# Optimization experiments

Measured on AMD Instinct MI355X. Metric: run time of the kernel, lower is better.

Reference implementation:

```python
import jax, jax.numpy as jnp
import numpy as np

N, E, G = 200000, 800000, 8192
IN, H, D, EXTRA = 128, 4, 64, 16


def setup_inputs() -> dict:
    key = jax.random.key(0)
    ks = jax.random.split(key, 24)
    inp = {
        'feats_node': jax.random.normal(ks[0], (N, IN), jnp.float32),
        'feats_graph': jax.random.normal(ks[1], (G, EXTRA), jnp.float32),
        'src': jax.random.randint(ks[2], (E,), 0, N, jnp.int32),
        'dst': jax.random.randint(ks[3], (E,), 0, N, jnp.int32),
        'graph_ids': jnp.sort(jax.random.randint(ks[4], (N,), 0, G, jnp.int32)),
        # GAT layer 1: fc [H*D, IN], attn [H, D], bias zeros (DGL default)
        'fc1_w': 0.5 * jax.random.normal(ks[5], (H * D, IN), jnp.float32),
        'attn_l1': 0.5 * jax.random.normal(ks[6], (H, D), jnp.float32),
        'attn_r1': 0.5 * jax.random.normal(ks[7], (H, D), jnp.float32),
        'bias1': jnp.zeros((H * D,), jnp.float32),
        # GAT layer 2
        'fc2_w': 0.5 * jax.random.normal(ks[8], (H * D, H * D), jnp.float32),
        'attn_l2': 0.5 * jax.random.normal(ks[9], (H, D), jnp.float32),
        'attn_r2': 0.5 * jax.random.normal(ks[10], (H, D), jnp.float32),
        'bias2': jnp.zeros((H * D,), jnp.float32),
        # GAT layer 3: 1 head
        'fc3_w': 0.5 * jax.random.normal(ks[11], (D, H * D), jnp.float32),
        'attn_l3': 0.5 * jax.random.normal(ks[12], (1, D), jnp.float32),
        'attn_r3': 0.5 * jax.random.normal(ks[13], (1, D), jnp.float32),
        'bias3': jnp.zeros((D,), jnp.float32),
        # readout score
        'score_w': 0.5 * jax.random.normal(ks[14], (1, D), jnp.float32),
        'score_b': jnp.zeros((1,), jnp.float32),
        # MLP: [D+EXTRA -> 2D -> D -> 1]
        'mlp_w1': 0.5 * jax.random.normal(ks[15], (2 * D, D + EXTRA), jnp.float32),
        'mlp_b1': jnp.zeros((2 * D,), jnp.float32),
        'mlp_w2': 0.5 * jax.random.normal(ks[16], (D, 2 * D), jnp.float32),
        'mlp_b2': jnp.zeros((D,), jnp.float32),
        'mlp_w3': 0.5 * jax.random.normal(ks[17], (1, D), jnp.float32),
        'mlp_b3': jnp.zeros((1,), jnp.float32),
    }
    return inp


def gat_conv(x, src, dst, fc_w, attn_l, attn_r, bias, n_heads, out_dim):
    # DGL GATConv: proj -> edge leaky_relu attention -> per-dst softmax -> aggregate
    n = x.shape[0]
    feat = (x @ fc_w.T).reshape(n, n_heads, out_dim)          # [N,H,D]
    el = jnp.einsum('nhd,hd->nh', feat, attn_l)               # [N,H]
    er = jnp.einsum('nhd,hd->nh', feat, attn_r)
    e = jax.nn.leaky_relu(el[src] + er[dst], 0.2)             # [E,H]
    m = jax.ops.segment_max(e, dst, num_segments=n)           # per-dst max
    m = jax.lax.stop_gradient(jnp.where(jnp.isfinite(m), m, 0.0))
    a = jnp.exp(e - m[dst])                                   # [E,H]
    denom = jax.ops.segment_sum(a, dst, num_segments=n)       # [N,H]
    alpha = a / jnp.where(denom[dst] == 0, 1.0, denom[dst])
    out = jax.ops.segment_sum(alpha[:, :, None] * feat[src], dst, num_segments=n)
    return out + bias.reshape(1, n_heads, out_dim)            # [N,H,D]


def reference(feats_node, feats_graph, src, dst, graph_ids,
              fc1_w, attn_l1, attn_r1, bias1,
              fc2_w, attn_l2, attn_r2, bias2,
              fc3_w, attn_l3, attn_r3, bias3,
              score_w, score_b,
              mlp_w1, mlp_b1, mlp_w2, mlp_b2, mlp_w3, mlp_b3):
    n = feats_node.shape[0]
    g = feats_graph.shape[0]
    x = jax.nn.selu(gat_conv(feats_node, src, dst, fc1_w, attn_l1, attn_r1, bias1, H, D)).reshape(n, H * D)
    x = jax.nn.selu(gat_conv(x, src, dst, fc2_w, attn_l2, attn_r2, bias2, H, D)).reshape(n, H * D)
    x = jax.nn.selu(gat_conv(x, src, dst, fc3_w, attn_l3, attn_r3, bias3, 1, D)).reshape(n, D)
    # weighted-average readout: sum(w*x)/sum(w) per graph
    w = jax.nn.sigmoid(x @ score_w.T + score_b)               # [N,1]
    num = jax.ops.segment_sum(w * x, graph_ids, num_segments=g)
    den = jax.ops.segment_sum(w, graph_ids, num_segments=g)
    emb = num / jnp.where(den == 0, 1.0, den)                 # [G,D]
    z = jnp.concatenate([emb, feats_graph], axis=1)           # [G,D+EXTRA]
    h = jax.nn.selu(z @ mlp_w1.T + mlp_b1)
    h = jax.nn.selu(h @ mlp_w2.T + mlp_b2)
    return h @ mlp_w3.T + mlp_b3                              # [G,1]
```

## Files before the change

### kernel.cpp

```cpp
#include <hip/hip_runtime.h>
#include <math.h>

#define N_NODES 200000
#define N_EDGES 800000
#define N_GRAPHS 8192
#define B1 16
#define B2G 16
#define EC2 128

typedef unsigned short ushort_t;

__device__ __forceinline__ float selu_f(float x){
  const float alpha = 1.6732632423543772f;
  const float lam   = 1.0507009873554805f;
  return x > 0.f ? lam * x : lam * alpha * (expf(x) - 1.f);
}
__device__ __forceinline__ float dot4(float4 a, float4 b){
  return a.x * b.x + a.y * b.y + a.z * b.z + a.w * b.w;
}

__global__ void zero_i32(int* p, int n){
  int i = blockIdx.x * 256 + threadIdx.x;
  if (i < n) p[i] = 0;
}

__global__ void deg_kernel(const int* __restrict__ dst, int* __restrict__ deg, int E){
  int e = blockIdx.x * 256 + threadIdx.x;
  if (e < E) atomicAdd(&deg[dst[e]], 1);
}

__global__ void scan1(const int* __restrict__ deg, int* __restrict__ rp, int* __restrict__ bs, int n){
  __shared__ int sh[256];
  int t = threadIdx.x;
  int base = blockIdx.x * 1024;
  int v[4]; int s = 0;
  #pragma unroll
  for (int i = 0; i < 4; i++){
    int idx = base + t * 4 + i;
    v[i] = (idx < n) ? deg[idx] : 0;
    s += v[i];
  }
  sh[t] = s; __syncthreads();
  for (int off = 1; off < 256; off <<= 1){
    int x = (t >= off) ? sh[t - off] : 0;
    __syncthreads();
    sh[t] += x;
    __syncthreads();
  }
  int run = (t == 0) ? 0 : sh[t - 1];
  #pragma unroll
  for (int i = 0; i < 4; i++){
    int idx = base + t * 4 + i;
    if (idx < n) rp[idx] = run;
    run += v[i];
  }
  if (t == 255) bs[blockIdx.x] = sh[255];
}

__global__ void scan2(int* bs, int nb){
  __shared__ int sh[256];
  int t = threadIdx.x;
  sh[t] = (t < nb) ? bs[t] : 0; __syncthreads();
  for (int off = 1; off < 256; off <<= 1){
    int x = (t >= off) ? sh[t - off] : 0;
    __syncthreads();
    sh[t] += x;
    __syncthreads();
  }
  int excl = (t == 0) ? 0 : sh[t - 1];
  if (t < nb) bs[t] = excl;
}

__global__ void scan3(int* rp, const int* __restrict__ bs, int n, int total){
  int i = blockIdx.x * 256 + threadIdx.x;
  if (i < n) rp[i] += bs[i >> 10];
  if (i == 0) rp[n] = total;
}

__global__ void fill_csr(const int* __restrict__ src, const int* __restrict__ dst,
                         const int* __restrict__ rp, int* __restrict__ fil,
                         int* __restrict__ csr, int E){
  int e = blockIdx.x * 256 + threadIdx.x;
  if (e < E){
    int d = dst[e];
    int p = atomicAdd(&fil[d], 1);
    csr[rp[d] + p] = src[e];
  }
}

__global__ void compute_v(const float* __restrict__ W1, const float* __restrict__ al1, const float* __restrict__ ar1,
                          const float* __restrict__ W2, const float* __restrict__ al2, const float* __restrict__ ar2,
                          const float* __restrict__ W3, const float* __restrict__ al3, const float* __restrict__ ar3,
                          float* __restrict__ V1L, float* __restrict__ V1R,
                          float* __restrict__ V2L, float* __restrict__ V2R,
                          float* __restrict__ V3L, float* __restrict__ V3R){
  int i = blockIdx.x * 256 + threadIdx.x;
  if (i < 512){
    int h = i >> 7, k = i & 127;
    float sl = 0.f, sr = 0.f;
    for (int dd = 0; dd < 64; dd++){
      float w = W1[(size_t)(h * 64 + dd) * 128 + k];
      sl += al1[h * 64 + dd] * w;
      sr += ar1[h * 64 + dd] * w;
    }
    V1L[i] = sl; V1R[i] = sr;
  } else if (i < 1536){
    int j = i - 512;
    int h = j >> 8, k = j & 255;
    float sl = 0.f, sr = 0.f;
    for (int dd = 0; dd < 64; dd++){
      float w = W2[(size_t)(h * 64 + dd) * 256 + k];
      sl += al2[h * 64 + dd] * w;
      sr += ar2[h * 64 + dd] * w;
    }
    V2L[j] = sl; V2R[j] = sr;
  } else if (i < 1792){
    int k = i - 1536;
    float sl = 0.f, sr = 0.f;
    for (int dd = 0; dd < 64; dd++){
      float w = W3[(size_t)dd * 256 + k];
      sl += al3[dd] * w;
      sr += ar3[dd] * w;
    }
    V3L[k] = sl; V3R[k] = sr;
  }
}

__global__ __launch_bounds__(256) void el_er1(const float* __restrict__ x0,
                                              const float* __restrict__ V1L, const float* __restrict__ V1R,
                                              float* __restrict__ el1, float* __restrict__ er1, int n){
  __shared__ float vl[512], vr[512];
  int t = threadIdx.x;
  for (int i = t; i < 512; i += 256){ vl[i] = V1L[i]; vr[i] = V1R[i]; }
  __syncthreads();
  int node = blockIdx.x * 4 + (t >> 6);
  int l = t & 63;
  if (node >= n) return;
  float xa = x0[(size_t)node * 128 + l];
  float xb = x0[(size_t)node * 128 + 64 + l];
  #pragma unroll
  for (int h = 0; h < 4; h++){
    float pl = xa * vl[h * 128 + l] + xb * vl[h * 128 + 64 + l];
    float pr = xa * vr[h * 128 + l] + xb * vr[h * 128 + 64 + l];
    #pragma unroll
    for (int off = 32; off; off >>= 1){ pl += __shfl_xor(pl, off); pr += __shfl_xor(pr, off); }
    if (l == 0){ el1[(size_t)node * 4 + h] = pl; er1[(size_t)node * 4 + h] = pr; }
  }
}

__global__ __launch_bounds__(256) void alpha_h4(const float* __restrict__ el, const float* __restrict__ er,
                                                const int* __restrict__ rp, const int* __restrict__ csr,
                                                float* __restrict__ a, int n){
  int node = blockIdx.x * 256 + threadIdx.x;
  if (node >= n) return;
  int s0 = rp[node], s1 = rp[node + 1];
  if (s0 >= s1) return;
  float4 erv = *reinterpret_cast<const float4*>(er + (size_t)node * 4);
  float m0 = -1e30f, m1 = -1e30f, m2 = -1e30f, m3 = -1e30f;
  for (int i = s0; i < s1; i++){
    float4 e = *reinterpret_cast<const float4*>(el + (size_t)csr[i] * 4);
    float e0 = e.x + erv.x; e0 = e0 > 0.f ? e0 : 0.2f * e0; m0 = fmaxf(m0, e0);
    float e1 = e.y + erv.y; e1 = e1 > 0.f ? e1 : 0.2f * e1; m1 = fmaxf(m1, e1);
    float e2 = e.z + erv.z; e2 = e2 > 0.f ? e2 : 0.2f * e2; m2 = fmaxf(m2, e2);
    float e3 = e.w + erv.w; e3 = e3 > 0.f ? e3 : 0.2f * e3; m3 = fmaxf(m3, e3);
  }
  float d0 = 0.f, d1 = 0.f, d2 = 0.f, d3 = 0.f;
  for (int i = s0; i < s1; i++){
    float4 e = *reinterpret_cast<const float4*>(el + (size_t)csr[i] * 4);
    float e0 = e.x + erv.x; e0 = e0 > 0.f ? e0 : 0.2f * e0; d0 += expf(e0 - m0);
    float e1 = e.y + erv.y; e1 = e1 > 0.f ? e1 : 0.2f * e1; d1 += expf(e1 - m1);
    float e2 = e.z + erv.z; e2 = e2 > 0.f ? e2 : 0.2f * e2; d2 += expf(e2 - m2);
    float e3 = e.w + erv.w; e3 = e3 > 0.f ? e3 : 0.2f * e3; d3 += expf(e3 - m3);
  }
  d0 = 1.f / d0; d1 = 1.f / d1; d2 = 1.f / d2; d3 = 1.f / d3;
  for (int i = s0; i < s1; i++){
    float4 e = *reinterpret_cast<const float4*>(el + (size_t)csr[i] * 4);
    float4 o;
    float e0 = e.x + erv.x; e0 = e0 > 0.f ? e0 : 0.2f * e0; o.x = expf(e0 - m0) * d0;
    float e1 = e.y + erv.y; e1 = e1 > 0.f ? e1 : 0.2f * e1; o.y = expf(e1 - m1) * d1;
    float e2 = e.z + erv.z; e2 = e2 > 0.f ? e2 : 0.2f * e2; o.z = expf(e2 - m2) * d2;
    float e3 = e.w + erv.w; e3 = e3 > 0.f ? e3 : 0.2f * e3; o.w = expf(e3 - m3) * d3;
    *reinterpret_cast<float4*>(a + (size_t)i * 4) = o;
  }
}

__global__ __launch_bounds__(256) void alpha_h1(const float* __restrict__ el, const float* __restrict__ er,
                                                const int* __restrict__ rp, const int* __restrict__ csr,
                                                float* __restrict__ a, int n){
  int node = blockIdx.x * 256 + threadIdx.x;
  if (node >= n) return;
  int s0 = rp[node], s1 = rp[node + 1];
  if (s0 >= s1) return;
  float erv = er[node];
  float m = -1e30f;
  for (int i = s0; i < s1; i++){
    float e = el[csr[i]] + erv; e = e > 0.f ? e : 0.2f * e; m = fmaxf(m, e);
  }
  float den = 0.f;
  for (int i = s0; i < s1; i++){
    float e = el[csr[i]] + erv; e = e > 0.f ? e : 0.2f * e; den += expf(e - m);
  }
  float inv = 1.f / den;
  for (int i = s0; i < s1; i++){
    float e = el[csr[i]] + erv; e = e > 0.f ? e : 0.2f * e; a[i] = expf(e - m) * inv;
  }
}

__global__ __launch_bounds__(512, 4) void l1_fused(
    const float* __restrict__ x0, const float* __restrict__ W1, const float* __restrict__ bias1,
    const float* __restrict__ a1, const float* __restrict__ W2,
    const float* __restrict__ V2L, const float* __restrict__ V2R,
    const int* __restrict__ rp, const int* __restrict__ csr,
    ushort_t* __restrict__ y1hi, unsigned char* __restrict__ y1lo,
    float* __restrict__ el2, float* __restrict__ er2){
  __shared__ float aggT[4][B1][132];
  __shared__ int rpc[B1 + 1];
  float* x1s = &aggT[0][0][0];
  int t = threadIdx.x;
  int nb0 = blockIdx.x * B1;
  if (t <= B1) rpc[t] = rp[nb0 + t];
  __syncthreads();

  {
    int g = t >> 5, c4 = t & 31;
    int i0 = rpc[g], i1 = rpc[g + 1];
    float acc[4][4] = {{0.f}};
    int s = (i0 < i1) ? csr[i0] : 0;
    for (int i = i0; i < i1; i++){
      int sn = (i + 1 < i1) ? csr[i + 1] : 0;
      float4 av = *reinterpret_cast<const float4*>(a1 + (size_t)i * 4);
      float4 xv = *reinterpret_cast<const float4*>(x0 + (size_t)s * 128 + c4 * 4);
      acc[0][0] += av.x * xv.x; acc[0][1] += av.x * xv.y; acc[0][2] += av.x * xv.z; acc[0][3] += av.x * xv.w;
      acc[1][0] += av.y * xv.x; acc[1][1] += av.y * xv.y; acc[1][2] += av.y * xv.z; acc[1][3] += av.y * xv.w;
      acc[2][0] += av.z * xv.x; acc[2][1] += av.z * xv.y; acc[2][2] += av.z * xv.z; acc[2][3] += av.z * xv.w;
      acc[3][0] += av.w * xv.x; acc[3][1] += av.w * xv.y; acc[3][2] += av.w * xv.z; acc[3][3] += av.w * xv.w;
      s = sn;
    }
    #pragma unroll
    for (int h = 0; h < 4; h++){
      float4 v = make_float4(acc[h][0], acc[h][1], acc[h][2], acc[h][3]);
      *reinterpret_cast<float4*>(&aggT[h][g][c4 * 4]) = v;
    }
  }
  __syncthreads();

  int mq = t >> 3, dg = t & 7;
  int m0 = mq * 4;
  int hh = mq >> 4;

  float acc1[4][2];
  {
    #pragma unroll
    for (int j = 0; j < 4; j++){ acc1[j][0] = 0.f; acc1[j][1] = 0.f; }
    const float* wp = W1 + (size_t)m0 * 128;
    #pragma unroll 2
    for (int kq = 0; kq < 32; kq++){
      int k = kq * 4;
      float4 w0 = *reinterpret_cast<const float4*>(wp + k);
      float4 w1 = *reinterpret_cast<const float4*>(wp + 128 + k);
      float4 w2 = *reinterpret_cast<const float4*>(wp + 256 + k);
      float4 w3 = *reinterpret_cast<const float4*>(wp + 384 + k);
      float4 a0 = *reinterpret_cast<const float4*>(&aggT[hh][dg][k]);
      float4 a1v = *reinterpret_cast<const float4*>(&aggT[hh][dg + 8][k]);
      acc1[0][0] += dot4(w0, a0); acc1[0][1] += dot4(w0, a1v);
      acc1[1][0] += dot4(w1, a0); acc1[1][1] += dot4(w1, a1v);
      acc1[2][0] += dot4(w2, a0); acc1[2][1] += dot4(w2, a1v);
      acc1[3][0] += dot4(w3, a0); acc1[3][1] += dot4(w3, a1v);
    }
  }
  __syncthreads();
  {
    float4 b = *reinterpret_cast<const float4*>(bias1 + m0);
    #pragma unroll
    for (int r = 0; r < 2; r++){
      int d = dg + 8 * r;
      float4 v;
      v.x = selu_f(acc1[0][r] + b.x);
      v.y = selu_f(acc1[1][r] + b.y);
      v.z = selu_f(acc1[2][r] + b.z);
      v.w = selu_f(acc1[3][r] + b.w);
      *reinterpret_cast<float4*>(&x1s[d * 260 + m0]) = v;
    }
  }
  __syncthreads();

  {
    float acc2[4][2];
    #pragma unroll
    for (int j = 0; j < 4; j++){ acc2[j][0] = 0.f; acc2[j][1] = 0.f; }
    const float* wp = W2 + (size_t)m0 * 256;
    #pragma unroll 2
    for (int kq = 0; kq < 64; kq++){
      int k = kq * 4;
      float4 w0 = *reinterpret_cast<const float4*>(wp + k);
      float4 w1 = *reinterpret_cast<const float4*>(wp + 256 + k);
      float4 w2 = *reinterpret_cast<const float4*>(wp + 512 + k);
      float4 w3 = *reinterpret_cast<const float4*>(wp + 768 + k);
      float4 x0v = *reinterpret_cast<const float4*>(&x1s[dg * 260 + k]);
      float4 x1v = *reinterpret_cast<const float4*>(&x1s[(dg + 8) * 260 + k]);
      acc2[0][0] += dot4(w0, x0v); acc2[0][1] += dot4(w0, x1v);
      acc2[1][0] += dot4(w1, x0v); acc2[1][1] += dot4(w1, x1v);
      acc2[2][0] += dot4(w2, x0v); acc2[2][1] += dot4(w2, x1v);
      acc2[3][0] += dot4(w3, x0v); acc2[3][1] += dot4(w3, x1v);
    }
    #pragma unroll
    for (int r = 0; r < 2; r++){
      int d = dg + 8 * r;
      unsigned int u0 = __float_as_uint(acc2[0][r]) + 0x80u;
      unsigned int u1 = __float_as_uint(acc2[1][r]) + 0x80u;
      unsigned int u2 = __float_as_uint(acc2[2][r]) + 0x80u;
      unsigned int u3 = __float_as_uint(acc2[3][r]) + 0x80u;
      ushort4 h4; uchar4 l4;
      h4.x = (ushort_t)(u0 >> 16); h4.y = (ushort_t)(u1 >> 16);
      h4.z = (ushort_t)(u2 >> 16); h4.w = (ushort_t)(u3 >> 16);
      l4.x = (unsigned char)(u0 >> 8); l4.y = (unsigned char)(u1 >> 8);
      l4.z = (unsigned char)(u2 >> 8); l4.w = (unsigned char)(u3 >> 8);
      size_t base = (size_t)(nb0 + d) * 256 + m0;
      *reinterpret_cast<ushort4*>(y1hi + base) = h4;
      *reinterpret_cast<uchar4*>(y1lo + base) = l4;
    }
  }

  if (t < 128){
    int d = t & 15, hq = (t >> 4) & 3, lr = t >> 6;
    const float* V = lr ? V2R : V2L;
    const float4* Vq = reinterpret_cast<const float4*>(V + hq * 256);
    const float4* Xq = reinterpret_cast<const float4*>(&x1s[d * 260]);
    float p = 0.f;
    #pragma unroll 4
    for (int q = 0; q < 64; q++){
      float4 v = Vq[q]; float4 x = Xq[q];
      p += v.x * x.x; p += v.y * x.y; p += v.z * x.z; p += v.w * x.w;
    }
    if (lr) er2[(size_t)(nb0 + d) * 4 + hq] = p;
    else    el2[(size_t)(nb0 + d) * 4 + hq] = p;
  }
}

__global__ __launch_bounds__(256, 4) void l2_gather(
    const ushort_t* __restrict__ y1hi, const unsigned char* __restrict__ y1lo,
    const float* __restrict__ bias2, const float* __restrict__ a2,
    const float* __restrict__ W3,
    const float* __restrict__ V3L, const float* __restrict__ V3R,
    const int* __restrict__ rp, const int* __restrict__ csr,
    float* __restrict__ feat3, float* __restrict__ el3, float* __restrict__ er3){
  __shared__ float x2s[B2G][257];
  __shared__ float W3c[16 * 257];
  __shared__ float als[EC2][4];
  __shared__ int   ssrc[EC2];
  __shared__ int   rpc[B2G + 1];
  int t = threadIdx.x;
  int nb0 = blockIdx.x * B2G;
  if (t <= B2G) rpc[t] = rp[nb0 + t];
  __syncthreads();
  int e0 = rpc[0], eN = rpc[B2G];
  int c = t;
  int h = c >> 6;

  float acc[B2G];
  #pragma unroll
  for (int d = 0; d < B2G; d++) acc[d] = 0.f;

  for (int c0 = e0; c0 < eN; c0 += EC2){
    int ce = min(EC2, eN - c0);
    for (int i = t; i < ce; i += 256){
      ssrc[i] = csr[c0 + i];
      float4 av = *reinterpret_cast<const float4*>(a2 + (size_t)(c0 + i) * 4);
      als[i][0] = av.x; als[i][1] = av.y; als[i][2] = av.z; als[i][3] = av.w;
    }
    __syncthreads();
    #pragma unroll
    for (int d = 0; d < B2G; d++){
      int lo = max(rpc[d], c0) - c0;
      int hi = min(rpc[d + 1], c0 + ce) - c0;
      for (int i = lo; i < hi; i++){
        size_t s = (size_t)ssrc[i] * 256 + c;
        unsigned int u = ((unsigned int)y1hi[s] << 16) | ((unsigned int)y1lo[s] << 8);
        acc[d] += als[i][h] * __uint_as_float(u);
      }
    }
    __syncthreads();
  }
  {
    float b = bias2[c];
    #pragma unroll
    for (int d = 0; d < B2G; d++) x2s[d][c] = selu_f(acc[d] + b);
  }
  __syncthreads();

  {
    int task = t >> 3, j = t & 7;
    int d = task & 15, lr = task >> 4;
    const float* V = lr ? V3R : V3L;
    float p = 0.f;
    for (int kk = 0; kk < 32; kk++){
      int k = j + kk * 8;
      p += V[k] * x2s[d][k];
    }
    p += __shfl_xor(p, 1); p += __shfl_xor(p, 2); p += __shfl_xor(p, 4);
    if (j == 0){ if (lr) er3[nb0 + d] = p; else el3[nb0 + d] = p; }
  }

  for (int ch = 0; ch < 4; ch++){
    __syncthreads();
    for (int i = t; i < 16 * 64; i += 256){
      int r = i >> 6, k4 = i & 63;
      float4 w = *reinterpret_cast<const float4*>(W3 + (size_t)(ch * 16 + r) * 256 + k4 * 4);
      W3c[r * 257 + k4 * 4 + 0] = w.x; W3c[r * 257 + k4 * 4 + 1] = w.y;
      W3c[r * 257 + k4 * 4 + 2] = w.z; W3c[r * 257 + k4 * 4 + 3] = w.w;
    }
    __syncthreads();
    {
      int r = t & 15, d = t >> 4;
      float s = 0.f;
      #pragma unroll 4
      for (int k = 0; k < 256; k++) s += W3c[r * 257 + k] * x2s[d][k];
      feat3[(size_t)(nb0 + d) * 64 + ch * 16 + r] = s;
    }
  }
}

__global__ __launch_bounds__(256) void gat_agg3(const float* __restrict__ feat, const float* __restrict__ a3,
                                                const int* __restrict__ rp, const int* __restrict__ csr,
                                                const float* __restrict__ bias,
                                                float* __restrict__ out, int n){
  int node = blockIdx.x * 4 + (threadIdx.x >> 6);
  int t = threadIdx.x & 63;
  if (node >= n) return;
  int s0 = rp[node], s1 = rp[node + 1];
  float acc = 0.f;
  for (int i = s0; i < s1; i += 4){
    float a[4], f[4];
    #pragma unroll
    for (int j = 0; j < 4; j++){
      int idx = i + j;
      bool vld = idx < s1;
      int idc = vld ? idx : s1 - 1;
      float av = a3[idc];
      if (!vld) av = 0.f;
      a[j] = av;
      f[j] = feat[(size_t)csr[idc] * 64 + t];
    }
    acc += a[0] * f[0] + a[1] * f[1] + a[2] * f[2] + a[3] * f[3];
  }
  out[(size_t)node * 64 + t] = selu_f(acc + bias[t]);
}

__global__ void readout_kernel(const float* __restrict__ x3, const float* __restrict__ score_w,
                               const float* __restrict__ score_b, const int* __restrict__ gids,
                               float* __restrict__ num, float* __restrict__ den, int n){
  int node = blockIdx.x * 4 + (threadIdx.x >> 6);
  int lane = threadIdx.x & 63;
  if (node >= n) return;
  float xv = x3[(size_t)node * 64 + lane];
  float p = xv * score_w[lane];
  #pragma unroll
  for (int off = 32; off; off >>= 1) p += __shfl_xor(p, off);
  float w = 1.f / (1.f + expf(-(p + score_b[0])));
  int g = gids[node];
  atomicAdd(&num[(size_t)g * 64 + lane], w * xv);
  if (lane == 0) atomicAdd(&den[g], w);
}

__global__ __launch_bounds__(128) void mlp_kernel(
    const float* __restrict__ num, const float* __restrict__ den,
    const float* __restrict__ fg,
    const float* __restrict__ w1, const float* __restrict__ b1,
    const float* __restrict__ w2, const float* __restrict__ b2,
    const float* __restrict__ w3, const float* __restrict__ b3,
    float* __restrict__ out, int G){
  __shared__ float z[80];
  __shared__ float h1[128];
  __shared__ float h2[64];
  int t = threadIdx.x;
  for (int g = blockIdx.x; g < G; g += gridDim.x){
    if (t < 64){
      float d = den[g];
      d = (d == 0.f) ? 1.f : d;
      z[t] = num[(size_t)g * 64 + t] / d;
    } else if (t < 80){
      z[t] = fg[(size_t)g * 16 + (t - 64)];
    }
    __syncthreads();
    {
      float a = b1[t];
      for (int k = 0; k < 80; k++) a += z[k] * w1[t * 80 + k];
      h1[t] = selu_f(a);
    }
    __syncthreads();
    if (t < 64){
      float a = b2[t];
      for (int k = 0; k < 128; k++) a += h1[k] * w2[t * 128 + k];
      h2[t] = selu_f(a);
    }
    __syncthreads();
    if (t < 64){
      float p = h2[t] * w3[t];
      #pragma unroll
      for (int off = 32; off; off >>= 1) p += __shfl_down(p, off);
      if (t == 0) out[g] = p + b3[0];
    }
    __syncthreads();
  }
}

extern "C" void kernel_launch(void* const* d_in, const int* in_sizes, int n_in,
                              void* d_out, int out_size, void* d_ws, size_t ws_size,
                              hipStream_t stream) {
  const float* feats_node  = (const float*)d_in[0];
  const float* feats_graph = (const float*)d_in[1];
  const int*   src         = (const int*)d_in[2];
  const int*   dst         = (const int*)d_in[3];
  const int*   gids        = (const int*)d_in[4];
  const float* fc1_w   = (const float*)d_in[5];
  const float* attn_l1 = (const float*)d_in[6];
  const float* attn_r1 = (const float*)d_in[7];
  const float* bias1   = (const float*)d_in[8];
  const float* fc2_w   = (const float*)d_in[9];
  const float* attn_l2 = (const float*)d_in[10];
  const float* attn_r2 = (const float*)d_in[11];
  const float* bias2   = (const float*)d_in[12];
  const float* fc3_w   = (const float*)d_in[13];
  const float* attn_l3 = (const float*)d_in[14];
  const float* attn_r3 = (const float*)d_in[15];
  const float* bias3   = (const float*)d_in[16];
  const float* score_w = (const float*)d_in[17];
  const float* score_b = (const float*)d_in[18];
  const float* mlp_w1  = (const float*)d_in[19];
  const float* mlp_b1  = (const float*)d_in[20];
  const float* mlp_w2  = (const float*)d_in[21];
  const float* mlp_b2  = (const float*)d_in[22];
  const float* mlp_w3  = (const float*)d_in[23];
  const float* mlp_b3  = (const float*)d_in[24];
  float* out = (float*)d_out;

  char* ws = (char*)d_ws;
  size_t off = 0;
  auto alloc = [&](size_t bytes) -> void* {
    void* p = ws + off;
    off += (bytes + 255) / 256 * 256;
    return p;
  };
  int*   deg   = (int*)alloc((size_t)N_NODES * 4);
  int*   fil   = (int*)alloc((size_t)N_NODES * 4);
  int*   rp    = (int*)alloc((size_t)(N_NODES + 1) * 4);
  int*   bs    = (int*)alloc(256 * 4);
  int*   csr   = (int*)alloc((size_t)N_EDGES * 4);
  float* elbuf = (float*)alloc((size_t)N_NODES * 4 * 4);
  float* erbuf = (float*)alloc((size_t)N_NODES * 4 * 4);
  float* V1L   = (float*)alloc(512 * 4);
  float* V1R   = (float*)alloc(512 * 4);
  float* V2L   = (float*)alloc(1024 * 4);
  float* V2R   = (float*)alloc(1024 * 4);
  float* V3L   = (float*)alloc(256 * 4);
  float* V3R   = (float*)alloc(256 * 4);
  float* num   = (float*)alloc((size_t)N_GRAPHS * 64 * 4);
  float* den   = (float*)alloc((size_t)N_GRAPHS * 4);
  float* A     = (float*)alloc((size_t)N_EDGES * 4 * 4);
  float* feat3 = (float*)alloc((size_t)N_NODES * 64 * 4);
  ushort_t*      y1hi = (ushort_t*)alloc((size_t)N_NODES * 256 * 2);
  unsigned char* y1lo = (unsigned char*)alloc((size_t)N_NODES * 256);
  float* x3 = (float*)y1hi;

  zero_i32<<<(N_NODES + 255) / 256, 256, 0, stream>>>(deg, N_NODES);
  zero_i32<<<(N_NODES + 255) / 256, 256, 0, stream>>>(fil, N_NODES);
  zero_i32<<<(N_GRAPHS * 64 + 255) / 256, 256, 0, stream>>>((int*)num, N_GRAPHS * 64);
  zero_i32<<<(N_GRAPHS + 255) / 256, 256, 0, stream>>>((int*)den, N_GRAPHS);

  deg_kernel<<<(N_EDGES + 255) / 256, 256, 0, stream>>>(dst, deg, N_EDGES);
  scan1<<<196, 256, 0, stream>>>(deg, rp, bs, N_NODES);
  scan2<<<1, 256, 0, stream>>>(bs, 196);
  scan3<<<(N_NODES + 255) / 256, 256, 0, stream>>>(rp, bs, N_NODES, N_EDGES);
  fill_csr<<<(N_EDGES + 255) / 256, 256, 0, stream>>>(src, dst, rp, fil, csr, N_EDGES);

  compute_v<<<7, 256, 0, stream>>>(fc1_w, attn_l1, attn_r1, fc2_w, attn_l2, attn_r2,
                                   fc3_w, attn_l3, attn_r3, V1L, V1R, V2L, V2R, V3L, V3R);
  el_er1<<<N_NODES / 4, 256, 0, stream>>>(feats_node, V1L, V1R, elbuf, erbuf, N_NODES);

  alpha_h4<<<(N_NODES + 255) / 256, 256, 0, stream>>>(elbuf, erbuf, rp, csr, A, N_NODES);
  l1_fused<<<N_NODES / B1, 512, 0, stream>>>(feats_node, fc1_w, bias1, A, fc2_w,
                                             V2L, V2R, rp, csr, y1hi, y1lo, elbuf, erbuf);
  alpha_h4<<<(N_NODES + 255) / 256, 256, 0, stream>>>(elbuf, erbuf, rp, csr, A, N_NODES);
  l2_gather<<<N_NODES / B2G, 256, 0, stream>>>(y1hi, y1lo, bias2, A, fc3_w,
                                               V3L, V3R, rp, csr, feat3, elbuf, erbuf);
  alpha_h1<<<(N_NODES + 255) / 256, 256, 0, stream>>>(elbuf, erbuf, rp, csr, A, N_NODES);
  gat_agg3<<<N_NODES / 4, 256, 0, stream>>>(feat3, A, rp, csr, bias3, x3, N_NODES);

  readout_kernel<<<N_NODES / 4, 256, 0, stream>>>(x3, score_w, score_b, gids, num, den, N_NODES);
  mlp_kernel<<<256, 128, 0, stream>>>(num, den, feats_graph,
                                      mlp_w1, mlp_b1, mlp_w2, mlp_b2, mlp_w3, mlp_b3,
                                      out, N_GRAPHS);
}
```

Baseline: 2.434 ms.

## Split layer-2 projection out of fused layer-1 kernel into separate GEMM kernel

The fc2 projection is moved out of the fused layer-1 kernel into a new kernel. The layer-1 kernel now writes the SELU activations in the split hi/lo 24-bit format, and y_transform reads them back, multiplies by W2 with a 32-node tile and 4x4 register blocking, and overwrites the buffer in place. This is meant to cut register pressure in the gather kernel and reuse each weight load across more nodes. The cost is an extra full round-trip of the 200000x256 activation buffer through global memory, plus an extra rounding of x1 before the projection.

```diff
diff --git a/kernel.cpp b/kernel.cpp
--- a/kernel.cpp
+++ b/kernel.cpp
@@ -206,12 +206,12 @@
   }
 }
 
-__global__ __launch_bounds__(512, 4) void l1_fused(
+__global__ __launch_bounds__(512, 4) void l1a(
     const float* __restrict__ x0, const float* __restrict__ W1, const float* __restrict__ bias1,
-    const float* __restrict__ a1, const float* __restrict__ W2,
+    const float* __restrict__ a1,
     const float* __restrict__ V2L, const float* __restrict__ V2R,
     const int* __restrict__ rp, const int* __restrict__ csr,
-    ushort_t* __restrict__ y1hi, unsigned char* __restrict__ y1lo,
+    ushort_t* __restrict__ zhi, unsigned char* __restrict__ zlo,
     float* __restrict__ el2, float* __restrict__ er2){
   __shared__ float aggT[4][B1][132];
   __shared__ int rpc[B1 + 1];
@@ -247,7 +247,6 @@
   int mq = t >> 3, dg = t & 7;
   int m0 = mq * 4;
   int hh = mq >> 4;
-
   float acc1[4][2];
   {
     #pragma unroll
@@ -285,39 +284,21 @@
   __syncthreads();
 
   {
-    float acc2[4][2];
-    #pragma unroll
-    for (int j = 0; j < 4; j++){ acc2[j][0] = 0.f; acc2[j][1] = 0.f; }
-    const float* wp = W2 + (size_t)m0 * 256;
-    #pragma unroll 2
-    for (int kq = 0; kq < 64; kq++){
-      int k = kq * 4;
-      float4 w0 = *reinterpret_cast<const float4*>(wp + k);
-      float4 w1 = *reinterpret_cast<const float4*>(wp + 256 + k);
-      float4 w2 = *reinterpret_cast<const float4*>(wp + 512 + k);
-      float4 w3 = *reinterpret_cast<const float4*>(wp + 768 + k);
-      float4 x0v = *reinterpret_cast<const float4*>(&x1s[dg * 260 + k]);
-      float4 x1v = *reinterpret_cast<const float4*>(&x1s[(dg + 8) * 260 + k]);
-      acc2[0][0] += dot4(w0, x0v); acc2[0][1] += dot4(w0, x1v);
-      acc2[1][0] += dot4(w1, x0v); acc2[1][1] += dot4(w1, x1v);
-      acc2[2][0] += dot4(w2, x0v); acc2[2][1] += dot4(w2, x1v);
-      acc2[3][0] += dot4(w3, x0v); acc2[3][1] += dot4(w3, x1v);
-    }
-    #pragma unroll
-    for (int r = 0; r < 2; r++){
-      int d = dg + 8 * r;
-      unsigned int u0 = __float_as_uint(acc2[0][r]) + 0x80u;
-      unsigned int u1 = __float_as_uint(acc2[1][r]) + 0x80u;
-      unsigned int u2 = __float_as_uint(acc2[2][r]) + 0x80u;
-      unsigned int u3 = __float_as_uint(acc2[3][r]) + 0x80u;
+    int row = t >> 5, cq = t & 31;
+    #pragma unroll
+    for (int it = 0; it < 2; it++){
+      int c4 = cq + it * 32;
+      float4 v = *reinterpret_cast<float4*>(&x1s[row * 260 + c4 * 4]);
+      unsigned int ux = __float_as_uint(v.x) + 0x80u, uy = __float_as_uint(v.y) + 0x80u;
+      unsigned int uz = __float_as_uint(v.z) + 0x80u, uw = __float_as_uint(v.w) + 0x80u;
       ushort4 h4; uchar4 l4;
-      h4.x = (ushort_t)(u0 >> 16); h4.y = (ushort_t)(u1 >> 16);
-      h4.z = (ushort_t)(u2 >> 16); h4.w = (ushort_t)(u3 >> 16);
-      l4.x = (unsigned char)(u0 >> 8); l4.y = (unsigned char)(u1 >> 8);
-      l4.z = (unsigned char)(u2 >> 8); l4.w = (unsigned char)(u3 >> 8);
-      size_t base = (size_t)(nb0 + d) * 256 + m0;
-      *reinterpret_cast<ushort4*>(y1hi + base) = h4;
-      *reinterpret_cast<uchar4*>(y1lo + base) = l4;
+      h4.x = (ushort_t)(ux >> 16); h4.y = (ushort_t)(uy >> 16);
+      h4.z = (ushort_t)(uz >> 16); h4.w = (ushort_t)(uw >> 16);
+      l4.x = (unsigned char)(ux >> 8); l4.y = (unsigned char)(uy >> 8);
+      l4.z = (unsigned char)(uz >> 8); l4.w = (unsigned char)(uw >> 8);
+      size_t base = (size_t)(nb0 + row) * 256 + c4 * 4;
+      *reinterpret_cast<ushort4*>(zhi + base) = h4;
+      *reinterpret_cast<uchar4*>(zlo + base) = l4;
     }
   }
 
@@ -334,6 +315,67 @@
     }
     if (lr) er2[(size_t)(nb0 + d) * 4 + hq] = p;
     else    el2[(size_t)(nb0 + d) * 4 + hq] = p;
+  }
+}
+
+__global__ __launch_bounds__(512, 4) void y_transform(
+    ushort_t* __restrict__ zhi, unsigned char* __restrict__ zlo,
+    const float* __restrict__ W2){
+  __shared__ float x1s[32 * 260];
+  int t = threadIdx.x;
+  int nb0 = blockIdx.x * 32;
+  for (int i = t; i < 32 * 64; i += 512){
+    int d = i >> 6, c4 = i & 63;
+    size_t base = (size_t)(nb0 + d) * 256 + c4 * 4;
+    ushort4 hv = *reinterpret_cast<const ushort4*>(zhi + base);
+    uchar4  lv = *reinterpret_cast<const uchar4*>(zlo + base);
+    float4 v;
+    v.x = __uint_as_float(((unsigned int)hv.x << 16) | ((unsigned int)lv.x << 8));
+    v.y = __uint_as_float(((unsigned int)hv.y << 16) | ((unsigned int)lv.y << 8));
+    v.z = __uint_as_float(((unsigned int)hv.z << 16) | ((unsigned int)lv.z << 8));
+    v.w = __uint_as_float(((unsigned int)hv.w << 16) | ((unsigned int)lv.w << 8));
+    *reinterpret_cast<float4*>(&x1s[d * 260 + c4 * 4]) = v;
+  }
+  __syncthreads();
+  int mq = t & 63, dgrp = t >> 6;
+  int m0 = mq * 4;
+  float acc[4][4];
+  #pragma unroll
+  for (int j = 0; j < 4; j++)
+    #pragma unroll
+    for (int r = 0; r < 4; r++) acc[j][r] = 0.f;
+  const float* wp = W2 + (size_t)m0 * 256;
+  #pragma unroll 2
+  for (int kq = 0; kq < 64; kq++){
+    int k = kq * 4;
+    float4 w0 = *reinterpret_cast<const float4*>(wp + k);
+    float4 w1 = *reinterpret_cast<const float4*>(wp + 256 + k);
+    float4 w2 = *reinterpret_cast<const float4*>(wp + 512 + k);
+    float4 w3 = *reinterpret_cast<const float4*>(wp + 768 + k);
+    #pragma unroll
+    for (int r = 0; r < 4; r++){
+      float4 xv = *reinterpret_cast<const float4*>(&x1s[(dgrp * 4 + r) * 260 + k]);
+      acc[0][r] += dot4(w0, xv);
+      acc[1][r] += dot4(w1, xv);
+      acc[2][r] += dot4(w2, xv);
+      acc[3][r] += dot4(w3, xv);
+    }
+  }
+  #pragma unroll
+  for (int r = 0; r < 4; r++){
+    int d = dgrp * 4 + r;
+    unsigned int u0 = __float_as_uint(acc[0][r]) + 0x80u;
+    unsigned int u1 = __float_as_uint(acc[1][r]) + 0x80u;
+    unsigned int u2 = __float_as_uint(acc[2][r]) + 0x80u;
+    unsigned int u3 = __float_as_uint(acc[3][r]) + 0x80u;
+    ushort4 h4; uchar4 l4;
+    h4.x = (ushort_t)(u0 >> 16); h4.y = (ushort_t)(u1 >> 16);
+    h4.z = (ushort_t)(u2 >> 16); h4.w = (ushort_t)(u3 >> 16);
+    l4.x = (unsigned char)(u0 >> 8); l4.y = (unsigned char)(u1 >> 8);
+    l4.z = (unsigned char)(u2 >> 8); l4.w = (unsigned char)(u3 >> 8);
+    size_t base = (size_t)(nb0 + d) * 256 + m0;
+    *reinterpret_cast<ushort4*>(zhi + base) = h4;
+    *reinterpret_cast<uchar4*>(zlo + base) = l4;
   }
 }
 
@@ -558,9 +600,9 @@
   float* den   = (float*)alloc((size_t)N_GRAPHS * 4);
   float* A     = (float*)alloc((size_t)N_EDGES * 4 * 4);
   float* feat3 = (float*)alloc((size_t)N_NODES * 64 * 4);
-  ushort_t*      y1hi = (ushort_t*)alloc((size_t)N_NODES * 256 * 2);
-  unsigned char* y1lo = (unsigned char*)alloc((size_t)N_NODES * 256);
-  float* x3 = (float*)y1hi;
+  ushort_t*      zhi = (ushort_t*)alloc((size_t)N_NODES * 256 * 2);
+  unsigned char* zlo = (unsigned char*)alloc((size_t)N_NODES * 256);
+  float* x3 = (float*)zhi;
 
   zero_i32<<<(N_NODES + 255) / 256, 256, 0, stream>>>(deg, N_NODES);
   zero_i32<<<(N_NODES + 255) / 256, 256, 0, stream>>>(fil, N_NODES);
@@ -578,10 +620,12 @@
   el_er1<<<N_NODES / 4, 256, 0, stream>>>(feats_node, V1L, V1R, elbuf, erbuf, N_NODES);
 
   alpha_h4<<<(N_NODES + 255) / 256, 256, 0, stream>>>(elbuf, erbuf, rp, csr, A, N_NODES);
-  l1_fused<<<N_NODES / B1, 512, 0, stream>>>(feats_node, fc1_w, bias1, A, fc2_w,
-                                             V2L, V2R, rp, csr, y1hi, y1lo, elbuf, erbuf);
+  l1a<<<N_NODES / B1, 512, 0, stream>>>(feats_node, fc1_w, bias1, A,
+                                        V2L, V2R, rp, csr, zhi, zlo, elbuf, erbuf);
+  y_transform<<<N_NODES / 32, 512, 0, stream>>>(zhi, zlo, fc2_w);
+
   alpha_h4<<<(N_NODES + 255) / 256, 256, 0, stream>>>(elbuf, erbuf, rp, csr, A, N_NODES);
-  l2_gather<<<N_NODES / B2G, 256, 0, stream>>>(y1hi, y1lo, bias2, A, fc3_w,
+  l2_gather<<<N_NODES / B2G, 256, 0, stream>>>(zhi, zlo, bias2, A, fc3_w,
                                                V3L, V3R, rp, csr, feat3, elbuf, erbuf);
   alpha_h1<<<(N_NODES + 255) / 256, 256, 0, stream>>>(elbuf, erbuf, rp, csr, A, N_NODES);
   gat_agg3<<<N_NODES / 4, 256, 0, stream>>>(feat3, A, rp, csr, bias3, x3, N_NODES);
```

After: 3.302 ms. 35.6% more time.
